# Kernel optimization log

Hardware: AMD Instinct MI355X
Metric: run time of the kernel (lower is better)

## Reference

```python
import jax, jax.numpy as jnp
import numpy as np

N_HEADS = 16
LOCAL_WINDOW = 256
GLOBAL_WINDOW = 1024


def _block_mha(x, in_proj_w, in_proj_b, out_proj_w, out_proj_b, window, n_heads):
    """Non-overlapping sliding-window MHA, matching torch nn.MultiheadAttention math.

    x: [B, S, D]; windows are independent -> fold them into the batch dim and do
    one batched attention (block-diagonal attention over the sequence).
    """
    B, S, D = x.shape
    nw = S // window
    hd = D // n_heads
    xw = x.reshape(B * nw, window, D)
    # combined QKV projection: in_proj_w is [3D, D], torch applies x @ W^T + b
    qkv = xw @ in_proj_w.T + in_proj_b  # [B*nw, W, 3D]
    q, k, v = jnp.split(qkv, 3, axis=-1)
    q = q.reshape(B * nw, window, n_heads, hd)
    k = k.reshape(B * nw, window, n_heads, hd)
    v = v.reshape(B * nw, window, n_heads, hd)
    scale = 1.0 / np.sqrt(hd).astype(np.float32)
    scores = jnp.einsum('bqhd,bkhd->bhqk', q, k) * scale
    attn = jax.nn.softmax(scores, axis=-1)
    out = jnp.einsum('bhqk,bkhd->bqhd', attn, v).reshape(B * nw, window, D)
    out = out @ out_proj_w.T + out_proj_b
    return out.reshape(B, S, D)


def setup_inputs() -> dict:
    key = jax.random.key(0)
    ks = jax.random.split(key, 8)
    B, S, D = 2, 4096, 1024
    w_scale = 1.0 / np.sqrt(D).astype(np.float32)
    return {
        'lqs': jax.random.normal(ks[0], (B, S, D), dtype=jnp.float32),
        'gqs': jax.random.normal(ks[1], (B, S, D), dtype=jnp.float32),
        'in_proj_w_l': jax.random.normal(ks[2], (3 * D, D), dtype=jnp.float32) * w_scale,
        'in_proj_b_l': jnp.zeros((3 * D,), dtype=jnp.float32),
        'out_proj_w_l': jax.random.normal(ks[3], (D, D), dtype=jnp.float32) * w_scale,
        'out_proj_b_l': jnp.zeros((D,), dtype=jnp.float32),
        'in_proj_w_g': jax.random.normal(ks[4], (3 * D, D), dtype=jnp.float32) * w_scale,
        'in_proj_b_g': jnp.zeros((3 * D,), dtype=jnp.float32),
        'out_proj_w_g': jax.random.normal(ks[5], (D, D), dtype=jnp.float32) * w_scale,
        'out_proj_b_g': jnp.zeros((D,), dtype=jnp.float32),
    }


def reference(lqs, gqs, in_proj_w_l, in_proj_b_l, out_proj_w_l, out_proj_b_l,
              in_proj_w_g, in_proj_b_g, out_proj_w_g, out_proj_b_g):
    local_out = _block_mha(lqs, in_proj_w_l, in_proj_b_l, out_proj_w_l, out_proj_b_l,
                           LOCAL_WINDOW, N_HEADS)
    global_out = _block_mha(gqs, in_proj_w_g, in_proj_b_g, out_proj_w_g, out_proj_b_g,
                            GLOBAL_WINDOW, N_HEADS)
    return (local_out, global_out)
```

## Files before the change

kernel.cpp:

```cpp
#include <hip/hip_runtime.h>
#include <stdint.h>

typedef __attribute__((ext_vector_type(8))) __bf16 bf16x8;
typedef __attribute__((ext_vector_type(4))) float f32x4;

__device__ __forceinline__ void async_ld16(const void* g, void* l) {
  __builtin_amdgcn_global_load_lds(
      (const __attribute__((address_space(1))) unsigned int*)g,
      (__attribute__((address_space(3))) unsigned int*)l, 16, 0, 0);
}

__device__ __forceinline__ unsigned short f2bf(float x) {
  union { float f; unsigned int u; } v; v.f = x;
  unsigned int r = v.u + 0x7FFFu + ((v.u >> 16) & 1u);
  return (unsigned short)(r >> 16);
}

__device__ __forceinline__ float exp2_fast(float x) {
  return __builtin_amdgcn_exp2f(x);
}

__device__ __forceinline__ unsigned int pack_bf2(float a, float b) {
  unsigned int ua = __builtin_bit_cast(unsigned int, a) + 0x8000u;
  unsigned int ub = __builtin_bit_cast(unsigned int, b) + 0x8000u;
  return __builtin_amdgcn_perm(ub, ua, 0x07060302u);
}

__global__ void cvt3(const float* __restrict__ x, unsigned short* __restrict__ xd,
                     const float* __restrict__ w1, unsigned short* __restrict__ w1d,
                     const float* __restrict__ w2, unsigned short* __restrict__ w2d) {
  int i = blockIdx.x * 256 + threadIdx.x;
  const float* s; unsigned short* d; int off;
  if (i < 2097152)      { s = x;  d = xd;  off = i; }
  else if (i < 2883584) { s = w1; d = w1d; off = i - 2097152; }
  else                  { s = w2; d = w2d; off = i - 2883584; }
  float4 v = ((const float4*)s)[off];
  ushort4 o;
  o.x = f2bf(v.x); o.y = f2bf(v.y); o.z = f2bf(v.z); o.w = f2bf(v.w);
  ((ushort4*)d)[off] = o;
}

__global__ __launch_bounds__(256)
void gemm_bt(const unsigned short* __restrict__ A0, const unsigned short* __restrict__ A1,
             const unsigned short* __restrict__ B0, const unsigned short* __restrict__ B1,
             const float* __restrict__ bias0, const float* __restrict__ bias1,
             void* __restrict__ out0, void* __restrict__ out1,
             int N, int K, int f32out, int qlim, float qs) {
  __shared__ unsigned short As[128 * 64];
  __shared__ unsigned short Bs[128 * 64];
  int br = blockIdx.z;
  const unsigned short* A = br ? A1 : A0;
  const unsigned short* B = br ? B1 : B0;
  const float* bias = br ? bias1 : bias0;
  void* outp = br ? out1 : out0;

  int tid = threadIdx.x;
  int wave = tid >> 6, lane = tid & 63;
  int quad = lane >> 4, l16 = lane & 15;
  int wm = (wave >> 1) * 64, wn = (wave & 1) * 64;
  size_t bm = (size_t)blockIdx.y * 128, bn = (size_t)blockIdx.x * 128;

  f32x4 zero = {0.f, 0.f, 0.f, 0.f};
  f32x4 acc[4][4];
  for (int i = 0; i < 4; i++)
    for (int j = 0; j < 4; j++) acc[i][j] = zero;

  int swz = l16 & 7;

  const unsigned short* ap[4];
#pragma unroll
  for (int j = 0; j < 4; j++) {
    int c = j * 256 + tid;
    int row = c >> 3, ss = (c & 7) ^ (row & 7);
    ap[j] = A + (bm + row) * K + ss * 8;
  }
  const ptrdiff_t dB = (B + bn * (size_t)K) - (A + bm * (size_t)K);

  for (int k0 = 0; k0 < K; k0 += 64) {
    __syncthreads();
#pragma unroll
    for (int j = 0; j < 4; j++) {
      int c = j * 256 + tid;
      async_ld16(ap[j],      (char*)As + c * 16);
      async_ld16(ap[j] + dB, (char*)Bs + c * 16);
      ap[j] += 64;
    }
    __syncthreads();

    bf16x8 bfr[4][2];
#pragma unroll
    for (int i = 0; i < 4; i++)
#pragma unroll
      for (int ch = 0; ch < 2; ch++) {
        int sl = (ch * 4 + quad) ^ swz;
        bfr[i][ch] = *(const bf16x8*)&Bs[(wn + i * 16 + l16) * 64 + sl * 8];
      }
#pragma unroll
    for (int mi = 0; mi < 4; mi++) {
      bf16x8 af[2];
#pragma unroll
      for (int ch = 0; ch < 2; ch++) {
        int sl = (ch * 4 + quad) ^ swz;
        af[ch] = *(const bf16x8*)&As[(wm + mi * 16 + l16) * 64 + sl * 8];
      }
#pragma unroll
      for (int ni = 0; ni < 4; ni++) {
        acc[mi][ni] = __builtin_amdgcn_mfma_f32_16x16x32_bf16(
            bfr[ni][0], af[0], acc[mi][ni], 0, 0, 0);
        acc[mi][ni] = __builtin_amdgcn_mfma_f32_16x16x32_bf16(
            bfr[ni][1], af[1], acc[mi][ni], 0, 0, 0);
      }
    }
  }

#pragma unroll
  for (int mi = 0; mi < 4; mi++) {
    size_t rowg = bm + wm + mi * 16 + l16;
#pragma unroll
    for (int ni = 0; ni < 4; ni++) {
      size_t col = bn + wn + ni * 16 + quad * 4;
      float s = ((int)col < qlim) ? qs : 1.0f;
      float4 bv = *(const float4*)&bias[col];
      f32x4 a = acc[mi][ni];
      if (f32out) {
        float4 o = {(a[0] + bv.x) * s, (a[1] + bv.y) * s,
                    (a[2] + bv.z) * s, (a[3] + bv.w) * s};
        *(float4*)&((float*)outp)[rowg * N + col] = o;
      } else {
        ushort4 o;
        o.x = f2bf((a[0] + bv.x) * s); o.y = f2bf((a[1] + bv.y) * s);
        o.z = f2bf((a[2] + bv.z) * s); o.w = f2bf((a[3] + bv.w) * s);
        *(ushort4*)&((unsigned short*)outp)[rowg * N + col] = o;
      }
    }
  }
}

__device__ __forceinline__ int kperm(int p) {
  return (p & 0xC3) | ((p & 0x0C) << 2) | ((p & 0x30) >> 2);
}
__global__ void transpose_v(const unsigned short* __restrict__ q0, unsigned short* __restrict__ v0, int W0,
                            const unsigned short* __restrict__ q1, unsigned short* __restrict__ v1, int W1,
                            int zsplit) {
  __shared__ unsigned short tile[64][33];
  int z = blockIdx.z;
  const unsigned short* qkv; unsigned short* vt; int W, wb, yy;
  if (z < zsplit) { qkv = q0; vt = v0; W = W0; wb = z; yy = blockIdx.y; }
  else { qkv = q1; vt = v1; W = W1; int t = z - zsplit; wb = t >> 2; yy = blockIdx.y + 4 * (t & 3); }
  int c0 = blockIdx.x * 32, w0 = yy * 64;
  const unsigned short* src = qkv + (size_t)wb * W * 3072 + 2048;
  for (int i = threadIdx.y; i < 64; i += 8)
    tile[i][threadIdx.x] = src[(size_t)(w0 + i) * 3072 + c0 + threadIdx.x];
  __syncthreads();
  unsigned short* dst = vt + (size_t)wb * 1024 * W;
  for (int i = threadIdx.y; i < 32; i += 8) {
    int p0 = threadIdx.x, p1 = threadIdx.x + 32;
    dst[(size_t)(c0 + i) * W + w0 + p0] = tile[kperm(p0)][i];
    dst[(size_t)(c0 + i) * W + w0 + p1] = tile[kperm(p1)][i];
  }
}

__global__ __launch_bounds__(256)
void attn_fused(const unsigned short* __restrict__ qkv0, const unsigned short* __restrict__ vt0,
                unsigned short* __restrict__ ao0, int W0, int nb0,
                const unsigned short* __restrict__ qkv1, const unsigned short* __restrict__ vt1,
                unsigned short* __restrict__ ao1, int W1) {
  __shared__ unsigned short Ks[64 * 64];
  __shared__ unsigned short Vs[64 * 64];
  __shared__ unsigned int   Ps[4][16 * 32];
  int bid = blockIdx.x;
  const unsigned short *qkv, *vtb0; unsigned short* ao; int W, rel;
  if (bid < nb0) { qkv = qkv0; vtb0 = vt0; ao = ao0; W = W0; rel = bid; }
  else           { qkv = qkv1; vtb0 = vt1; ao = ao1; W = W1; rel = bid - nb0; }
  int gx = W >> 7;
  int shift = (gx == 2) ? 1 : 3;
  int bx = rel & (gx - 1);
  int wbh = rel >> shift;
  int wb = wbh >> 4, h = wbh & 15;

  int tid = threadIdx.x;
  int wave = tid >> 6, lane = tid & 63;
  int quad = lane >> 4, l16 = lane & 15;
  int swz = l16 & 7;
  int q0w = bx * 128 + wave * 32;

  const unsigned short* qb = qkv + (size_t)wb * W * 3072 + h * 64;
  const unsigned short* kb = qb + 1024;
  const unsigned short* vtb = vtb0 + (size_t)wbh * 64 * W;

  bf16x8 qf[2][2];
  for (int cb = 0; cb < 2; cb++)
    for (int ch = 0; ch < 2; ch++)
      qf[cb][ch] = *(const bf16x8*)(qb + (size_t)(q0w + cb * 16 + l16) * 3072 +
                                    ch * 32 + quad * 8);

  f32x4 zero = {0.f, 0.f, 0.f, 0.f};
  f32x4 O[2][4];
  for (int cb = 0; cb < 2; cb++)
    for (int g = 0; g < 4; g++) O[cb][g] = zero;
  float l_i[2] = {0.f, 0.f};

  for (int k0 = 0; k0 < W; k0 += 64) {
    __syncthreads();
    for (int j = 0; j < 2; j++) {
      int c = j * 256 + tid;
      int row = c >> 3, sl = c & 7, ss = sl ^ (row & 7);
      async_ld16(kb + (size_t)(k0 + row) * 3072 + ss * 8, (char*)Ks + c * 16);
      async_ld16(vtb + (size_t)row * W + k0 + ss * 8,     (char*)Vs + c * 16);
    }
    __syncthreads();

    bf16x8 ak[4][2], vf[4][2];
#pragma unroll
    for (int i = 0; i < 4; i++)
#pragma unroll
      for (int ch = 0; ch < 2; ch++) {
        int sl = (ch * 4 + quad) ^ swz;
        ak[i][ch] = *(const bf16x8*)&Ks[(i * 16 + l16) * 64 + sl * 8];
        vf[i][ch] = *(const bf16x8*)&Vs[(i * 16 + l16) * 64 + sl * 8];
      }

    for (int cb = 0; cb < 2; cb++) {
      unsigned int pk[8];
      float sm = 0.f;
#pragma unroll
      for (int sub = 0; sub < 4; sub++) {
        f32x4 z = zero;
        z = __builtin_amdgcn_mfma_f32_16x16x32_bf16(ak[sub][0], qf[cb][0], z, 0, 0, 0);
        z = __builtin_amdgcn_mfma_f32_16x16x32_bf16(ak[sub][1], qf[cb][1], z, 0, 0, 0);
        float p0 = exp2_fast(z[0]), p1 = exp2_fast(z[1]);
        float p2 = exp2_fast(z[2]), p3 = exp2_fast(z[3]);
        sm += (p0 + p1) + (p2 + p3);
        pk[((sub & 1) * 2) + (sub >> 1) * 4]     = pack_bf2(p0, p1);
        pk[((sub & 1) * 2) + (sub >> 1) * 4 + 1] = pack_bf2(p2, p3);
      }
      sm += __shfl_xor(sm, 16);
      sm += __shfl_xor(sm, 32);
      l_i[cb] += sm;

      unsigned int* pw = &Ps[wave][0];
      uint4 u0 = {pk[0], pk[1], pk[2], pk[3]};
      uint4 u1 = {pk[4], pk[5], pk[6], pk[7]};
      *(uint4*)&pw[l16 * 32 + ((2 * quad) ^ swz) * 4]     = u0;
      *(uint4*)&pw[l16 * 32 + ((2 * quad + 1) ^ swz) * 4] = u1;

      bf16x8 pf[2];
#pragma unroll
      for (int ch = 0; ch < 2; ch++) {
        uint4 u = *(const uint4*)&pw[l16 * 32 + ((ch * 4 + quad) ^ swz) * 4];
        pf[ch] = __builtin_bit_cast(bf16x8, u);
      }
#pragma unroll
      for (int g = 0; g < 4; g++) {
        O[cb][g] = __builtin_amdgcn_mfma_f32_16x16x32_bf16(pf[0], vf[g][0], O[cb][g], 0, 0, 0);
        O[cb][g] = __builtin_amdgcn_mfma_f32_16x16x32_bf16(pf[1], vf[g][1], O[cb][g], 0, 0, 0);
      }
    }
  }

  for (int cb = 0; cb < 2; cb++) {
    float inv = 1.0f / l_i[cb];
    float ivr[4];
    for (int r = 0; r < 4; r++) ivr[r] = __shfl(inv, quad * 4 + r);
    for (int r = 0; r < 4; r++) {
      size_t rowg = (size_t)wb * W + q0w + cb * 16 + quad * 4 + r;
      for (int g = 0; g < 4; g++)
        ao[rowg * 1024 + h * 64 + g * 16 + l16] = f2bf(O[cb][g][r] * ivr[r]);
    }
  }
}

extern "C" void kernel_launch(void* const* d_in, const int* in_sizes, int n_in,
                              void* d_out, int out_size, void* d_ws, size_t ws_size,
                              hipStream_t stream) {
  const int D = 1024, TD = 3072, M = 8192;
  const float QS = 0.125f * 1.44269504089f;
  const size_t PER = 46137344;
  bool comb = ws_size >= (size_t)2 * PER * 2;

  unsigned short* Xb[2]; unsigned short* Wb[2]; unsigned short* Ob[2];
  unsigned short* qkv[2]; unsigned short* vt[2];
  for (int b = 0; b < 2; b++) {
    unsigned short* base = (unsigned short*)d_ws + (comb ? b * PER : 0);
    Xb[b]  = base;
    Wb[b]  = Xb[b] + 8388608;
    Ob[b]  = Wb[b] + 3145728;
    qkv[b] = Ob[b] + 1048576;
    vt[b]  = qkv[b] + 25165824;
  }
  float* outp = (float*)d_out;
  const float* x[2]   = {(const float*)d_in[0], (const float*)d_in[1]};
  const float* ipw[2] = {(const float*)d_in[2], (const float*)d_in[6]};
  const float* ipb[2] = {(const float*)d_in[3], (const float*)d_in[7]};
  const float* opw[2] = {(const float*)d_in[4], (const float*)d_in[8]};
  const float* opb[2] = {(const float*)d_in[5], (const float*)d_in[9]};
  const int Wd[2] = {256, 1024};

  if (comb) {
    for (int b = 0; b < 2; b++)
      cvt3<<<12288, 256, 0, stream>>>(x[b], Xb[b], ipw[b], Wb[b], opw[b], Ob[b]);
    gemm_bt<<<dim3(TD / 128, M / 128, 2), 256, 0, stream>>>(
        Xb[0], Xb[1], Wb[0], Wb[1], ipb[0], ipb[1], qkv[0], qkv[1],
        TD, D, 0, D, QS);
    transpose_v<<<dim3(32, 4, 64), dim3(32, 8), 0, stream>>>(
        qkv[0], vt[0], 256, qkv[1], vt[1], 1024, 32);
    attn_fused<<<2048, 256, 0, stream>>>(
        qkv[0], vt[0], Xb[0], 256, 1024, qkv[1], vt[1], Xb[1], 1024);
    gemm_bt<<<dim3(D / 128, M / 128, 2), 256, 0, stream>>>(
        Xb[0], Xb[1], Ob[0], Ob[1], opb[0], opb[1], outp, outp + 8388608,
        D, D, 1, 0, 1.0f);
  } else {
    for (int b = 0; b < 2; b++) {
      int W = Wd[b], nwb = M / W;
      cvt3<<<12288, 256, 0, stream>>>(x[b], Xb[b], ipw[b], Wb[b], opw[b], Ob[b]);
      gemm_bt<<<dim3(TD / 128, M / 128, 1), 256, 0, stream>>>(
          Xb[b], Xb[b], Wb[b], Wb[b], ipb[b], ipb[b], qkv[b], qkv[b],
          TD, D, 0, D, QS);
      if (b == 0)
        transpose_v<<<dim3(32, 4, 32), dim3(32, 8), 0, stream>>>(
            qkv[b], vt[b], W, qkv[b], vt[b], W, 32);
      else
        transpose_v<<<dim3(32, 4, 32), dim3(32, 8), 0, stream>>>(
            qkv[b], vt[b], W, qkv[b], vt[b], W, 0);
      int nb = (W >> 7) * nwb * 16;
      attn_fused<<<nb, 256, 0, stream>>>(
          qkv[b], vt[b], Xb[b], W, nb, qkv[b], vt[b], Xb[b], W);
      gemm_bt<<<dim3(D / 128, M / 128, 1), 256, 0, stream>>>(
          Xb[b], Xb[b], Ob[b], Ob[b], opb[b], opb[b],
          outp + (size_t)b * 8388608, outp + (size_t)b * 8388608,
          D, D, 1, 0, 1.0f);
    }
  }
}
```

Baseline: 456.0 us.

## Rewrite bf16 GEMM with 256x256 tiles, 8 waves and double-buffered async LDS pipeline

The projection GEMM moves from a 128x128 tile with 4 waves and a single LDS buffer to a 256x256 tile with 8 waves, split-K halves and double-buffered LDS. Global-to-LDS async loads for the next tiles are interleaved with MFMA blocks, with barriers, wave priority boosts and explicit vmcnt waits. Each output element gets more data reuse, and memory latency is meant to be hidden behind compute. In exchange it uses more registers (8x4 accumulators per wave) and 64KB of LDS, and launches fewer blocks, so the QKV and output GEMMs may fill fewer CUs.

```diff
diff --git a/kernel.cpp b/kernel.cpp
--- a/kernel.cpp
+++ b/kernel.cpp
@@ -40,14 +40,14 @@
   ((ushort4*)d)[off] = o;
 }
 
-__global__ __launch_bounds__(256)
+__global__ __launch_bounds__(512, 2)
 void gemm_bt(const unsigned short* __restrict__ A0, const unsigned short* __restrict__ A1,
              const unsigned short* __restrict__ B0, const unsigned short* __restrict__ B1,
              const float* __restrict__ bias0, const float* __restrict__ bias1,
              void* __restrict__ out0, void* __restrict__ out1,
              int N, int K, int f32out, int qlim, float qs) {
-  __shared__ unsigned short As[128 * 64];
-  __shared__ unsigned short Bs[128 * 64];
+  __shared__ unsigned short As[2][2][256 * 32];
+  __shared__ unsigned short Bs[2][2][256 * 32];
   int br = blockIdx.z;
   const unsigned short* A = br ? A1 : A0;
   const unsigned short* B = br ? B1 : B0;
@@ -57,64 +57,111 @@
   int tid = threadIdx.x;
   int wave = tid >> 6, lane = tid & 63;
   int quad = lane >> 4, l16 = lane & 15;
-  int wm = (wave >> 1) * 64, wn = (wave & 1) * 64;
-  size_t bm = (size_t)blockIdx.y * 128, bn = (size_t)blockIdx.x * 128;
-
+  int wm = (wave >> 2) * 128;
+  int wn = (wave & 3) * 64;
+  size_t bm = (size_t)blockIdx.y * 256, bn = (size_t)blockIdx.x * 256;
+
+  f32x4 acc[8][4];
   f32x4 zero = {0.f, 0.f, 0.f, 0.f};
-  f32x4 acc[4][4];
-  for (int i = 0; i < 4; i++)
+#pragma unroll
+  for (int i = 0; i < 8; i++)
+#pragma unroll
     for (int j = 0; j < 4; j++) acc[i][j] = zero;
 
-  int swz = l16 & 7;
-
-  const unsigned short* ap[4];
-#pragma unroll
-  for (int j = 0; j < 4; j++) {
-    int c = j * 256 + tid;
-    int row = c >> 3, ss = (c & 7) ^ (row & 7);
-    ap[j] = A + (bm + row) * K + ss * 8;
-  }
-  const ptrdiff_t dB = (B + bn * (size_t)K) - (A + bm * (size_t)K);
-
-  for (int k0 = 0; k0 < K; k0 += 64) {
-    __syncthreads();
-#pragma unroll
-    for (int j = 0; j < 4; j++) {
-      int c = j * 256 + tid;
-      async_ld16(ap[j],      (char*)As + c * 16);
-      async_ld16(ap[j] + dB, (char*)Bs + c * 16);
-      ap[j] += 64;
-    }
-    __syncthreads();
-
-    bf16x8 bfr[4][2];
-#pragma unroll
-    for (int i = 0; i < 4; i++)
-#pragma unroll
-      for (int ch = 0; ch < 2; ch++) {
-        int sl = (ch * 4 + quad) ^ swz;
-        bfr[i][ch] = *(const bf16x8*)&Bs[(wn + i * 16 + l16) * 64 + sl * 8];
-      }
-#pragma unroll
-    for (int mi = 0; mi < 4; mi++) {
-      bf16x8 af[2];
-#pragma unroll
-      for (int ch = 0; ch < 2; ch++) {
-        int sl = (ch * 4 + quad) ^ swz;
-        af[ch] = *(const bf16x8*)&As[(wm + mi * 16 + l16) * 64 + sl * 8];
-      }
-#pragma unroll
-      for (int ni = 0; ni < 4; ni++) {
-        acc[mi][ni] = __builtin_amdgcn_mfma_f32_16x16x32_bf16(
-            bfr[ni][0], af[0], acc[mi][ni], 0, 0, 0);
-        acc[mi][ni] = __builtin_amdgcn_mfma_f32_16x16x32_bf16(
-            bfr[ni][1], af[1], acc[mi][ni], 0, 0, 0);
-      }
-    }
-  }
-
-#pragma unroll
-  for (int mi = 0; mi < 4; mi++) {
+  int swc = (quad ^ ((l16 >> 1) & 3)) * 16;
+  const char* ArdB = (const char*)As + (wm + l16) * 64 + swc;
+  const char* BrdB = (const char*)Bs + (wn + l16) * 64 + swc;
+
+  int row0 = tid >> 2, c0 = (tid & 3) ^ ((row0 >> 1) & 3);
+  int row1 = row0 + 128, c1 = (tid & 3) ^ ((row1 >> 1) & 3);
+  const char* Ag0 = (const char*)(A + (bm + row0) * (size_t)K) + c0 * 16;
+  const char* Ag1 = (const char*)(A + (bm + row1) * (size_t)K) + c1 * 16;
+  const char* Bg0 = (const char*)(B + (bn + row0) * (size_t)K) + c0 * 16;
+  const char* Bg1 = (const char*)(B + (bn + row1) * (size_t)K) + c1 * 16;
+  char* ldsA = (char*)As + tid * 16;
+  char* ldsB = (char*)Bs + tid * 16;
+
+#define STAGE_A(po_, kh_, koff_) do {                    \
+    char* d_ = ldsA + (po_) + (kh_) * 16384;             \
+    async_ld16(Ag0 + (koff_), d_);                       \
+    async_ld16(Ag1 + (koff_), d_ + 8192); } while (0)
+#define STAGE_B(po_, kh_, koff_) do {                    \
+    char* d_ = ldsB + (po_) + (kh_) * 16384;             \
+    async_ld16(Bg0 + (koff_), d_);                       \
+    async_ld16(Bg1 + (koff_), d_ + 8192); } while (0)
+#define LDA_F(po_, kh_, mi_) (*(const bf16x8*)(ArdB + (po_) + (kh_) * 16384 + (mi_) * 1024))
+#define LDB_F(po_, kh_, ni_) (*(const bf16x8*)(BrdB + (po_) + (kh_) * 16384 + (ni_) * 1024))
+#define BAR() do { __builtin_amdgcn_s_barrier(); __builtin_amdgcn_sched_barrier(0); } while (0)
+#define MFMAQ(mb_) do {                                                                              \
+    acc[(mb_)+0][0] = __builtin_amdgcn_mfma_f32_16x16x32_bf16(b0, a0, acc[(mb_)+0][0], 0, 0, 0);     \
+    acc[(mb_)+1][0] = __builtin_amdgcn_mfma_f32_16x16x32_bf16(b0, a1, acc[(mb_)+1][0], 0, 0, 0);     \
+    acc[(mb_)+2][0] = __builtin_amdgcn_mfma_f32_16x16x32_bf16(b0, a2, acc[(mb_)+2][0], 0, 0, 0);     \
+    acc[(mb_)+3][0] = __builtin_amdgcn_mfma_f32_16x16x32_bf16(b0, a3, acc[(mb_)+3][0], 0, 0, 0);     \
+    acc[(mb_)+0][1] = __builtin_amdgcn_mfma_f32_16x16x32_bf16(b1, a0, acc[(mb_)+0][1], 0, 0, 0);     \
+    acc[(mb_)+1][1] = __builtin_amdgcn_mfma_f32_16x16x32_bf16(b1, a1, acc[(mb_)+1][1], 0, 0, 0);     \
+    acc[(mb_)+2][1] = __builtin_amdgcn_mfma_f32_16x16x32_bf16(b1, a2, acc[(mb_)+2][1], 0, 0, 0);     \
+    acc[(mb_)+3][1] = __builtin_amdgcn_mfma_f32_16x16x32_bf16(b1, a3, acc[(mb_)+3][1], 0, 0, 0);     \
+    acc[(mb_)+0][2] = __builtin_amdgcn_mfma_f32_16x16x32_bf16(b2, a0, acc[(mb_)+0][2], 0, 0, 0);     \
+    acc[(mb_)+1][2] = __builtin_amdgcn_mfma_f32_16x16x32_bf16(b2, a1, acc[(mb_)+1][2], 0, 0, 0);     \
+    acc[(mb_)+2][2] = __builtin_amdgcn_mfma_f32_16x16x32_bf16(b2, a2, acc[(mb_)+2][2], 0, 0, 0);     \
+    acc[(mb_)+3][2] = __builtin_amdgcn_mfma_f32_16x16x32_bf16(b2, a3, acc[(mb_)+3][2], 0, 0, 0);     \
+    acc[(mb_)+0][3] = __builtin_amdgcn_mfma_f32_16x16x32_bf16(b3, a0, acc[(mb_)+0][3], 0, 0, 0);     \
+    acc[(mb_)+1][3] = __builtin_amdgcn_mfma_f32_16x16x32_bf16(b3, a1, acc[(mb_)+1][3], 0, 0, 0);     \
+    acc[(mb_)+2][3] = __builtin_amdgcn_mfma_f32_16x16x32_bf16(b3, a2, acc[(mb_)+2][3], 0, 0, 0);     \
+    acc[(mb_)+3][3] = __builtin_amdgcn_mfma_f32_16x16x32_bf16(b3, a3, acc[(mb_)+3][3], 0, 0, 0);     \
+  } while (0)
+
+  const int NT = K >> 6;
+
+  STAGE_A(0, 0, 0);       STAGE_B(0, 0, 0);
+  STAGE_A(0, 1, 64);      STAGE_B(0, 1, 64);
+  STAGE_A(32768, 0, 128); STAGE_B(32768, 0, 128);
+  asm volatile("s_waitcnt vmcnt(4)" ::: "memory");
+  BAR();
+
+  for (int j = 0; j < NT; ++j) {
+    int po = (j & 1) * 32768;
+    int qo = po ^ 32768;
+    int t1 = (j + 1 < NT) ? j + 1 : NT - 1;
+    int t2 = (j + 2 < NT) ? j + 2 : NT - 1;
+    int ko1 = t1 * 128 + 64;
+    int ko2 = t2 * 128;
+    bf16x8 a0, a1, a2, a3, b0, b1, b2, b3;
+
+    b0 = LDB_F(po, 0, 0); b1 = LDB_F(po, 0, 1); b2 = LDB_F(po, 0, 2); b3 = LDB_F(po, 0, 3);
+    a0 = LDA_F(po, 0, 0); a1 = LDA_F(po, 0, 1); a2 = LDA_F(po, 0, 2); a3 = LDA_F(po, 0, 3);
+    STAGE_A(qo, 1, ko1);
+    BAR();
+    __builtin_amdgcn_s_setprio(1); MFMAQ(0); __builtin_amdgcn_s_setprio(0);
+    BAR();
+    a0 = LDA_F(po, 0, 4); a1 = LDA_F(po, 0, 5); a2 = LDA_F(po, 0, 6); a3 = LDA_F(po, 0, 7);
+    STAGE_B(qo, 1, ko1);
+    BAR();
+    __builtin_amdgcn_s_setprio(1); MFMAQ(4); __builtin_amdgcn_s_setprio(0);
+    BAR();
+    b0 = LDB_F(po, 1, 0); b1 = LDB_F(po, 1, 1); b2 = LDB_F(po, 1, 2); b3 = LDB_F(po, 1, 3);
+    a0 = LDA_F(po, 1, 0); a1 = LDA_F(po, 1, 1); a2 = LDA_F(po, 1, 2); a3 = LDA_F(po, 1, 3);
+    STAGE_A(po, 0, ko2);
+    BAR();
+    __builtin_amdgcn_s_setprio(1); MFMAQ(0); __builtin_amdgcn_s_setprio(0);
+    BAR();
+    a0 = LDA_F(po, 1, 4); a1 = LDA_F(po, 1, 5); a2 = LDA_F(po, 1, 6); a3 = LDA_F(po, 1, 7);
+    STAGE_B(po, 0, ko2);
+    BAR();
+    __builtin_amdgcn_s_setprio(1); MFMAQ(4); __builtin_amdgcn_s_setprio(0);
+    asm volatile("s_waitcnt vmcnt(4)" ::: "memory");
+    BAR();
+  }
+
+#undef STAGE_A
+#undef STAGE_B
+#undef LDA_F
+#undef LDB_F
+#undef BAR
+#undef MFMAQ
+
+#pragma unroll
+  for (int mi = 0; mi < 8; mi++) {
     size_t rowg = bm + wm + mi * 16 + l16;
 #pragma unroll
     for (int ni = 0; ni < 4; ni++) {
@@ -299,21 +346,21 @@
   if (comb) {
     for (int b = 0; b < 2; b++)
       cvt3<<<12288, 256, 0, stream>>>(x[b], Xb[b], ipw[b], Wb[b], opw[b], Ob[b]);
-    gemm_bt<<<dim3(TD / 128, M / 128, 2), 256, 0, stream>>>(
+    gemm_bt<<<dim3(TD / 256, M / 256, 2), 512, 0, stream>>>(
         Xb[0], Xb[1], Wb[0], Wb[1], ipb[0], ipb[1], qkv[0], qkv[1],
         TD, D, 0, D, QS);
     transpose_v<<<dim3(32, 4, 64), dim3(32, 8), 0, stream>>>(
         qkv[0], vt[0], 256, qkv[1], vt[1], 1024, 32);
     attn_fused<<<2048, 256, 0, stream>>>(
         qkv[0], vt[0], Xb[0], 256, 1024, qkv[1], vt[1], Xb[1], 1024);
-    gemm_bt<<<dim3(D / 128, M / 128, 2), 256, 0, stream>>>(
+    gemm_bt<<<dim3(D / 256, M / 256, 2), 512, 0, stream>>>(
         Xb[0], Xb[1], Ob[0], Ob[1], opb[0], opb[1], outp, outp + 8388608,
         D, D, 1, 0, 1.0f);
   } else {
     for (int b = 0; b < 2; b++) {
       int W = Wd[b], nwb = M / W;
       cvt3<<<12288, 256, 0, stream>>>(x[b], Xb[b], ipw[b], Wb[b], opw[b], Ob[b]);
-      gemm_bt<<<dim3(TD / 128, M / 128, 1), 256, 0, stream>>>(
+      gemm_bt<<<dim3(TD / 256, M / 256, 1), 512, 0, stream>>>(
           Xb[b], Xb[b], Wb[b], Wb[b], ipb[b], ipb[b], qkv[b], qkv[b],
           TD, D, 0, D, QS);
       if (b == 0)
@@ -325,7 +372,7 @@
       int nb = (W >> 7) * nwb * 16;
       attn_fused<<<nb, 256, 0, stream>>>(
           qkv[b], vt[b], Xb[b], W, nb, qkv[b], vt[b], Xb[b], W);
-      gemm_bt<<<dim3(D / 128, M / 128, 1), 256, 0, stream>>>(
+      gemm_bt<<<dim3(D / 256, M / 256, 1), 512, 0, stream>>>(
           Xb[b], Xb[b], Ob[b], Ob[b], opb[b], opb[b],
           outp + (size_t)b * 8388608, outp + (size_t)b * 8388608,
           D, D, 1, 0, 1.0f);
```

Result: faster. 425.6 us (-6.7%).
